# Performance work log

Hardware: AMD Instinct MI355X
Metric: run time of the kernel (lower is better)

Reference implementation:

```python
import jax, jax.numpy as jnp
import numpy as np

N = 10000       # nodes
E = 640000      # edges (before self-loops)
D_IN = 128
H1 = 128
H2 = 64
EMB = 64
NEG_SLOPE = 0.2  # PyG GATConv default


def setup_inputs() -> dict:
    key = jax.random.key(0)
    ks = jax.random.split(key, 12)
    s = 0.05
    return {
        "x": jax.random.normal(ks[0], (N, D_IN), dtype=jnp.float32),
        "edge_index": jax.random.randint(ks[1], (2, E), 0, N, dtype=jnp.int64),
        "W1": jax.random.normal(ks[2], (D_IN, H1), dtype=jnp.float32) * s,
        "a_src1": jax.random.normal(ks[3], (H1,), dtype=jnp.float32) * s,
        "a_dst1": jax.random.normal(ks[4], (H1,), dtype=jnp.float32) * s,
        "b1": jnp.zeros((H1,), dtype=jnp.float32),
        "W2": jax.random.normal(ks[5], (H1, H2), dtype=jnp.float32) * s,
        "a_src2": jax.random.normal(ks[6], (H2,), dtype=jnp.float32) * s,
        "a_dst2": jax.random.normal(ks[7], (H2,), dtype=jnp.float32) * s,
        "b2": jnp.zeros((H2,), dtype=jnp.float32),
        "Wp": jax.random.normal(ks[8], (H2, EMB), dtype=jnp.float32) * s,
        "bp": jnp.zeros((EMB,), dtype=jnp.float32),
    }


def _gat_conv(x, src, dst, W, a_src, a_dst, b):
    # x: [N, Din] -> h: [N, Dout]
    h = x @ W
    # edge-wise attention logits (PyG: alpha_src from source j, alpha_dst from target i)
    logits = jax.nn.leaky_relu((h @ a_src)[src] + (h @ a_dst)[dst], NEG_SLOPE)  # [E+N]
    # softmax over incoming edges of each destination node (numerically stable)
    m = jax.ops.segment_max(logits, dst, num_segments=N)
    e = jnp.exp(logits - m[dst])
    z = jax.ops.segment_sum(e, dst, num_segments=N)
    w = e / z[dst]                                                              # [E+N]
    # weighted scatter-add of source features into destinations
    out = jax.ops.segment_sum(w[:, None] * h[src], dst, num_segments=N)         # [N, Dout]
    return out + b


def reference(x, edge_index, W1, a_src1, a_dst1, b1, W2, a_src2, a_dst2, b2, Wp, bp):
    # add self-loops (PyG GATConv default add_self_loops=True)
    loop = jnp.arange(N, dtype=edge_index.dtype)
    ei = jnp.concatenate([edge_index, jnp.stack([loop, loop])], axis=1)
    src, dst = ei[0], ei[1]
    x1 = jax.nn.relu(_gat_conv(x, src, dst, W1, a_src1, a_dst1, b1))
    x2 = jax.nn.relu(_gat_conv(x1, src, dst, W2, a_src2, a_dst2, b2))
    return x2 @ Wp + bp  # [N, EMB]
```

## Files before the change

kernel.cpp:

```cpp
#include <hip/hip_runtime.h>
#include <hip/hip_bf16.h>

#define NNODES 10000
#define NEDGES 640000
#define NTOT   (NNODES + NEDGES)
#define D_IN 128
#define H1 128
#define H2 64
#define EMB 64

#define NBUCKET 160
#define BCAP    8192
#define CHUNK   4096


__global__ __launch_bounds__(256) void bucket_kernel(const int* __restrict__ ei,
                                                     int* __restrict__ bucket_cursor,
                                                     int* __restrict__ bucket_arr) {
    __shared__ int ordered[CHUNK];
    __shared__ int hist[NBUCKET];
    __shared__ int binStart[NBUCKET];
    __shared__ int bincur[NBUCKET];
    __shared__ int gcur[NBUCKET];
    __shared__ int wtmp[4];

    int tid = threadIdx.x;
    int base = blockIdx.x * CHUNK;
    int n = NTOT - base; if (n > CHUNK) n = CHUNK;

    int rec[CHUNK / 256];
#pragma unroll
    for (int k = 0; k < CHUNK / 256; ++k) {
        int i = base + k * 256 + tid;
        int r = 0;
        if (i < NTOT) {
            int s, d;
            if (i < NEDGES) { s = ei[i]; d = ei[NEDGES + i]; }
            else            { s = d = i - NEDGES; }
            r = (d << 16) | s;
        }
        rec[k] = r;
    }

    for (int b = tid; b < NBUCKET; b += 256) hist[b] = 0;
    __syncthreads();
#pragma unroll
    for (int k = 0; k < CHUNK / 256; ++k) {
        int i = base + k * 256 + tid;
        if (i < NTOT) atomicAdd(&hist[rec[k] >> 22], 1);
    }
    __syncthreads();

    {
        int v = (tid < NBUCKET) ? hist[tid] : 0;
        int lane = tid & 63, w = tid >> 6;
        int inc = v;
        for (int o = 1; o < 64; o <<= 1) {
            int t = __shfl_up(inc, o, 64);
            if (lane >= o) inc += t;
        }
        if (lane == 63) wtmp[w] = inc;
        __syncthreads();
        int pre = 0;
        for (int i = 0; i < w; ++i) pre += wtmp[i];
        if (tid < NBUCKET) {
            binStart[tid] = pre + inc - v;
            bincur[tid]   = pre + inc - v;
        }
    }
    __syncthreads();

#pragma unroll
    for (int k = 0; k < CHUNK / 256; ++k) {
        int i = base + k * 256 + tid;
        if (i < NTOT) {
            int pos = atomicAdd(&bincur[rec[k] >> 22], 1);
            ordered[pos] = rec[k];
        }
    }
    __syncthreads();

    for (int b = tid; b < NBUCKET; b += 256) {
        int c = hist[b];
        gcur[b] = c ? atomicAdd(&bucket_cursor[b], c) : 0;
    }
    __syncthreads();

#pragma unroll
    for (int k = 0; k < CHUNK / 256; ++k) {
        int i = k * 256 + tid;
        if (i < n) {
            int r = ordered[i];
            int b = r >> 22;
            bucket_arr[b * BCAP + gcur[b] + (i - binStart[b])] = r;
        }
    }
}

__global__ __launch_bounds__(256) void bucket_scan_kernel(const int* __restrict__ bucket_cursor,
                                                          int* __restrict__ bucket_base) {
    __shared__ int wtmp[4];
    int tid = threadIdx.x;
    int v = (tid < NBUCKET) ? bucket_cursor[tid] : 0;
    int lane = tid & 63, w = tid >> 6;
    int inc = v;
    for (int o = 1; o < 64; o <<= 1) {
        int t = __shfl_up(inc, o, 64);
        if (lane >= o) inc += t;
    }
    if (lane == 63) wtmp[w] = inc;
    __syncthreads();
    int pre = 0;
    for (int i = 0; i < w; ++i) pre += wtmp[i];
    if (tid < NBUCKET) bucket_base[tid] = pre + inc - v;
}


__global__ __launch_bounds__(256) void build_kernel(const int* __restrict__ bucket_cursor,
                                                    const int* __restrict__ bucket_base,
                                                    const int* __restrict__ bucket_arr,
                                                    int* __restrict__ rowptr,
                                                    int* __restrict__ csr_src) {
    __shared__ int hist[64];
    __shared__ int bincur[64];
    int tid = threadIdx.x;
    int b = blockIdx.x;
    int cnt = bucket_cursor[b];
    int base = bucket_base[b];
    const int* arr = bucket_arr + b * BCAP;

    if (tid < 64) hist[tid] = 0;
    __syncthreads();
    for (int i = tid; i < cnt; i += 256) atomicAdd(&hist[(arr[i] >> 16) & 63], 1);
    __syncthreads();

    if (tid < 64) {
        int v = hist[tid];
        int inc = v;
        for (int o = 1; o < 64; o <<= 1) {
            int t = __shfl_up(inc, o, 64);
            if (tid >= o) inc += t;
        }
        bincur[tid] = inc - v;
        int node = b * 64 + tid;
        if (node < NNODES) rowptr[node] = base + inc - v;
    }
    if (b == 0 && tid == 0) rowptr[NNODES] = NTOT;
    __syncthreads();

    for (int i = tid; i < cnt; i += 256) {
        int r = arr[i];
        int pos = base + atomicAdd(&bincur[(r >> 16) & 63], 1);
        csr_src[pos] = r & 0xFFFF;
    }
}


template <int K, int NC, bool BIAS, bool DOTS>
__global__ __launch_bounds__(256) void gemm_kernel(const float* __restrict__ A,
                                                   const float* __restrict__ B,
                                                   const float* __restrict__ bias,
                                                   float* __restrict__ C, int M,
                                                   const float* __restrict__ a_src,
                                                   const float* __restrict__ a_dst,
                                                   float* __restrict__ as,
                                                   float* __restrict__ ad) {
    __shared__ float Alds[32 * K];
    __shared__ float Blds[K * NC];
    int tid = threadIdx.x;
    int row0 = blockIdx.x * 32;

    const float4* A4 = (const float4*)(A + (size_t)row0 * K);
    float4* Al4 = (float4*)Alds;
    constexpr int A4N = 32 * K / 4;
    for (int idx = tid; idx < A4N; idx += 256) {
        int r = idx / (K / 4);
        float4 z4 = {0.f, 0.f, 0.f, 0.f};
        Al4[idx] = (row0 + r < M) ? A4[idx] : z4;
    }
    const float4* B4 = (const float4*)B;
    float4* Bl4 = (float4*)Blds;
    constexpr int B4N = K * NC / 4;
    for (int idx = tid; idx < B4N; idx += 256) Bl4[idx] = B4[idx];
    __syncthreads();

    int tx = tid & 31;
    int ty = tid >> 5;
    constexpr int CPT = NC / 32;
    float acc[4][CPT];
#pragma unroll
    for (int rr = 0; rr < 4; ++rr)
#pragma unroll
        for (int cc = 0; cc < CPT; ++cc) acc[rr][cc] = 0.f;

    for (int k = 0; k < K; ++k) {
        float bv[CPT];
        const float* Bk = &Blds[k * NC + tx * CPT];
#pragma unroll
        for (int cc = 0; cc < CPT; ++cc) bv[cc] = Bk[cc];
#pragma unroll
        for (int rr = 0; rr < 4; ++rr) {
            float a = Alds[(ty + 8 * rr) * K + k];
#pragma unroll
            for (int cc = 0; cc < CPT; ++cc) acc[rr][cc] = fmaf(a, bv[cc], acc[rr][cc]);
        }
    }

#pragma unroll
    for (int rr = 0; rr < 4; ++rr) {
        int gr = row0 + ty + 8 * rr;
        if (gr < M) {
#pragma unroll
            for (int cc = 0; cc < CPT; ++cc) {
                int c = tx * CPT + cc;
                float v = acc[rr][cc];
                if (BIAS) v += bias[c];
                C[(size_t)gr * NC + c] = v;
            }
        }
    }

    if (DOTS) {
        float asv[CPT], adv[CPT];
#pragma unroll
        for (int cc = 0; cc < CPT; ++cc) {
            asv[cc] = a_src[tx * CPT + cc];
            adv[cc] = a_dst[tx * CPT + cc];
        }
#pragma unroll
        for (int rr = 0; rr < 4; ++rr) {
            float s1 = 0.f, s2 = 0.f;
#pragma unroll
            for (int cc = 0; cc < CPT; ++cc) {
                s1 = fmaf(acc[rr][cc], asv[cc], s1);
                s2 = fmaf(acc[rr][cc], adv[cc], s2);
            }
#pragma unroll
            for (int o = 1; o < 32; o <<= 1) {
                s1 += __shfl_xor(s1, o, 64);
                s2 += __shfl_xor(s2, o, 64);
            }
            int gr = row0 + ty + 8 * rr;
            if (tx == 0 && gr < M) { as[gr] = s1; ad[gr] = s2; }
        }
    }
}


template <int H>
__global__ __launch_bounds__(256) void agg_kernel(const int* __restrict__ rowptr,
                                                  const int* __restrict__ csr_src,
                                                  const float* __restrict__ h,
                                                  const float* __restrict__ as,
                                                  const float* __restrict__ ad,
                                                  const float* __restrict__ bias,
                                                  float* __restrict__ out) {
    int wid = (blockIdx.x * blockDim.x + threadIdx.x) >> 6;
    int lane = threadIdx.x & 63;
    if (wid >= NNODES) return;
    int beg = rowptr[wid];
    int end = rowptr[wid + 1];
    float ad_d = ad[wid];

    const float2* h2 = (const float2*)h;
    float z = 0.f, acc0 = 0.f, acc1 = 0.f;

    for (int chunk = beg; chunk < end; chunk += 64) {
        int myj = chunk + lane;
        int cnt = end - chunk; if (cnt > 64) cnt = 64;
        int s_l = 0;
        float e_l = 0.f;
        if (myj < end) {
            s_l = csr_src[myj];
            float l = as[s_l] + ad_d;
            l = (l > 0.f) ? l : 0.2f * l;
            e_l = __expf(l);
        }
        z += e_l;
        int cnt4 = (cnt + 3) & ~3;
        for (int t = 0; t < cnt4; t += 4) {
#pragma unroll
            for (int u = 0; u < 4; ++u) {
                int tt = __builtin_amdgcn_readfirstlane(t + u);
                int s = __builtin_amdgcn_readlane(s_l, tt);
                float e = __int_as_float(
                    __builtin_amdgcn_readlane(__float_as_int(e_l), tt));
                if (H == 128) {
                    float2 v = h2[(size_t)s * 64 + lane];
                    acc0 = fmaf(e, v.x, acc0);
                    acc1 = fmaf(e, v.y, acc1);
                } else {
                    float v = h[(size_t)s * H + lane];
                    acc0 = fmaf(e, v, acc0);
                }
            }
        }
    }
    for (int o = 32; o; o >>= 1) z += __shfl_xor(z, o, 64);
    float rz = 1.f / z;
    if (H == 128) {
        float2 bb = ((const float2*)bias)[lane];
        float2 o2;
        o2.x = fmaxf(acc0 * rz + bb.x, 0.f);
        o2.y = fmaxf(acc1 * rz + bb.y, 0.f);
        ((float2*)out)[(size_t)wid * 64 + lane] = o2;
    } else {
        float o0 = fmaxf(acc0 * rz + bias[lane], 0.f);
        out[(size_t)wid * H + lane] = o0;
    }
}


extern "C" void kernel_launch(void* const* d_in, const int* in_sizes, int n_in,
                              void* d_out, int out_size, void* d_ws, size_t ws_size,
                              hipStream_t stream) {
    const float* x      = (const float*)d_in[0];
    const int*   ei     = (const int*)d_in[1];
    const float* W1     = (const float*)d_in[2];
    const float* a_src1 = (const float*)d_in[3];
    const float* a_dst1 = (const float*)d_in[4];
    const float* b1     = (const float*)d_in[5];
    const float* W2     = (const float*)d_in[6];
    const float* a_src2 = (const float*)d_in[7];
    const float* a_dst2 = (const float*)d_in[8];
    const float* b2     = (const float*)d_in[9];
    const float* Wp     = (const float*)d_in[10];
    const float* bp     = (const float*)d_in[11];
    float* out = (float*)d_out;

    char* ws = (char*)d_ws;
    size_t off = 0;
    auto alloc = [&](size_t bytes) {
        void* p = ws + off;
        off = (off + bytes + 255) & ~(size_t)255;
        return p;
    };
    int*   bucket_cursor = (int*)alloc(NBUCKET * 4);
    int*   bucket_base   = (int*)alloc(NBUCKET * 4);
    int*   bucket_arr    = (int*)alloc((size_t)NBUCKET * BCAP * 4);
    int*   rowptr  = (int*)alloc((NNODES + 1) * 4);
    int*   csr_src = (int*)alloc((size_t)NTOT * 4);
    float* h1      = (float*)alloc((size_t)NNODES * H1 * 4);
    float* as1     = (float*)alloc(NNODES * 4);
    float* ad1     = (float*)alloc(NNODES * 4);
    float* x1      = (float*)alloc((size_t)NNODES * H1 * 4);
    float* h2      = (float*)alloc((size_t)NNODES * H2 * 4);
    float* as2     = (float*)alloc(NNODES * 4);
    float* ad2     = (float*)alloc(NNODES * 4);
    float* x2      = (float*)alloc((size_t)NNODES * H2 * 4);
    (void)ws_size;

    const int TB = 256;
    int gemm_b = (NNODES + 31) / 32;
    int wave_b = (NNODES * 64 + TB - 1) / TB;
    int p1_b = (NTOT + CHUNK - 1) / CHUNK;

    hipMemsetAsync(bucket_cursor, 0, NBUCKET * 4, stream);
    bucket_kernel<<<p1_b, TB, 0, stream>>>(ei, bucket_cursor, bucket_arr);
    bucket_scan_kernel<<<1, TB, 0, stream>>>(bucket_cursor, bucket_base);
    build_kernel<<<NBUCKET - 3, TB, 0, stream>>>(bucket_cursor, bucket_base,
                                                 bucket_arr, rowptr, csr_src);

    gemm_kernel<D_IN, H1, false, true><<<gemm_b, TB, 0, stream>>>(
        x, W1, nullptr, h1, NNODES, a_src1, a_dst1, as1, ad1);
    agg_kernel<H1><<<wave_b, TB, 0, stream>>>(rowptr, csr_src, h1, as1, ad1, b1, x1);

    gemm_kernel<H1, H2, false, true><<<gemm_b, TB, 0, stream>>>(
        x1, W2, nullptr, h2, NNODES, a_src2, a_dst2, as2, ad2);
    agg_kernel<H2><<<wave_b, TB, 0, stream>>>(rowptr, csr_src, h2, as2, ad2, b2, x2);

    gemm_kernel<H2, EMB, true, false><<<gemm_b, TB, 0, stream>>>(
        x2, Wp, bp, out, NNODES, nullptr, nullptr, nullptr, nullptr);
}
```

Before: 184.3 us.

## Fuse all stages into one persistent kernel with grid-wide barriers

Replaces the chain of separate launches (bucket, scan, build, three GEMMs, two aggregations) with one persistent 256-block kernel that uses atomic grid barriers between phases. The first layer's GEMM runs on spare blocks at the same time as edge bucketing, and the bucket scan is folded into the build phase. GEMM tiles now stream K in 64-wide slices so all phases can share one shared-memory union. This removes launch gaps and tail effects, but limits parallelism to 256 blocks, relies on all blocks being co-resident for the spin barriers, and shared-memory use may lower occupancy.

```diff
diff --git a/kernel.cpp b/kernel.cpp
--- a/kernel.cpp
+++ b/kernel.cpp
@@ -12,20 +12,45 @@
 #define NBUCKET 160
 #define BCAP    8192
 #define CHUNK   4096
-
-
-__global__ __launch_bounds__(256) void bucket_kernel(const int* __restrict__ ei,
-                                                     int* __restrict__ bucket_cursor,
-                                                     int* __restrict__ bucket_arr) {
-    __shared__ int ordered[CHUNK];
-    __shared__ int hist[NBUCKET];
-    __shared__ int binStart[NBUCKET];
-    __shared__ int bincur[NBUCKET];
-    __shared__ int gcur[NBUCKET];
-    __shared__ int wtmp[4];
-
+#define NCHUNK  ((NTOT + CHUNK - 1) / CHUNK)
+#define NTILE   ((NNODES + 31) / 32)
+#define NBBLK   ((NNODES + 63) / 64)
+#define GRID    256
+#define TB      256
+
+struct Params {
+    const float* x; const int* ei;
+    const float* W1; const float* a_src1; const float* a_dst1; const float* b1;
+    const float* W2; const float* a_src2; const float* a_dst2; const float* b2;
+    const float* Wp; const float* bp;
+    float* out;
+    int* bar; int* bucket_cursor; int* bucket_arr; int* rowptr; int* csr_src;
+    float* h1; float* as1; float* ad1; float* x1;
+    float* h2; float* as2; float* ad2; float* x2;
+};
+
+union SMem {
+    struct { int ordered[CHUNK]; int hist[NBUCKET]; int binStart[NBUCKET];
+             int bincur[NBUCKET]; int gcur[NBUCKET]; int wtmp[4]; } p1;
+    struct { int base[NBUCKET]; int wtmp[4]; int hist[64]; int bincur[64]; } p2;
+    struct { float A[32 * 64]; float B[64 * 128]; } g;
+};
+
+__device__ __forceinline__ void gridbar(int* __restrict__ bar, int k) {
+    __syncthreads();
+    if (threadIdx.x == 0) {
+        __hip_atomic_fetch_add(&bar[k], 1, __ATOMIC_RELEASE, __HIP_MEMORY_SCOPE_AGENT);
+        while (__hip_atomic_load(&bar[k], __ATOMIC_ACQUIRE, __HIP_MEMORY_SCOPE_AGENT) < GRID)
+            __builtin_amdgcn_s_sleep(2);
+    }
+    __syncthreads();
+}
+
+__device__ __forceinline__ void bucket_chunk(SMem& sm, int c, const int* __restrict__ ei,
+                                             int* __restrict__ bucket_cursor,
+                                             int* __restrict__ bucket_arr) {
     int tid = threadIdx.x;
-    int base = blockIdx.x * CHUNK;
+    int base = c * CHUNK;
     int n = NTOT - base; if (n > CHUNK) n = CHUNK;
 
     int rec[CHUNK / 256];
@@ -42,30 +67,30 @@
         rec[k] = r;
     }
 
-    for (int b = tid; b < NBUCKET; b += 256) hist[b] = 0;
+    for (int b = tid; b < NBUCKET; b += 256) sm.p1.hist[b] = 0;
     __syncthreads();
 #pragma unroll
     for (int k = 0; k < CHUNK / 256; ++k) {
         int i = base + k * 256 + tid;
-        if (i < NTOT) atomicAdd(&hist[rec[k] >> 22], 1);
+        if (i < NTOT) atomicAdd(&sm.p1.hist[rec[k] >> 22], 1);
     }
     __syncthreads();
 
     {
-        int v = (tid < NBUCKET) ? hist[tid] : 0;
+        int v = (tid < NBUCKET) ? sm.p1.hist[tid] : 0;
         int lane = tid & 63, w = tid >> 6;
         int inc = v;
         for (int o = 1; o < 64; o <<= 1) {
             int t = __shfl_up(inc, o, 64);
             if (lane >= o) inc += t;
         }
-        if (lane == 63) wtmp[w] = inc;
+        if (lane == 63) sm.p1.wtmp[w] = inc;
         __syncthreads();
         int pre = 0;
-        for (int i = 0; i < w; ++i) pre += wtmp[i];
+        for (int i = 0; i < w; ++i) pre += sm.p1.wtmp[i];
         if (tid < NBUCKET) {
-            binStart[tid] = pre + inc - v;
-            bincur[tid]   = pre + inc - v;
+            sm.p1.binStart[tid] = pre + inc - v;
+            sm.p1.bincur[tid]   = pre + inc - v;
         }
     }
     __syncthreads();
@@ -74,15 +99,15 @@
     for (int k = 0; k < CHUNK / 256; ++k) {
         int i = base + k * 256 + tid;
         if (i < NTOT) {
-            int pos = atomicAdd(&bincur[rec[k] >> 22], 1);
-            ordered[pos] = rec[k];
+            int pos = atomicAdd(&sm.p1.bincur[rec[k] >> 22], 1);
+            sm.p1.ordered[pos] = rec[k];
         }
     }
     __syncthreads();
 
     for (int b = tid; b < NBUCKET; b += 256) {
-        int c = hist[b];
-        gcur[b] = c ? atomicAdd(&bucket_cursor[b], c) : 0;
+        int cc = sm.p1.hist[b];
+        sm.p1.gcur[b] = cc ? atomicAdd(&bucket_cursor[b], cc) : 0;
     }
     __syncthreads();
 
@@ -90,58 +115,51 @@
     for (int k = 0; k < CHUNK / 256; ++k) {
         int i = k * 256 + tid;
         if (i < n) {
-            int r = ordered[i];
+            int r = sm.p1.ordered[i];
             int b = r >> 22;
-            bucket_arr[b * BCAP + gcur[b] + (i - binStart[b])] = r;
-        }
-    }
-}
-
-__global__ __launch_bounds__(256) void bucket_scan_kernel(const int* __restrict__ bucket_cursor,
-                                                          int* __restrict__ bucket_base) {
-    __shared__ int wtmp[4];
+            bucket_arr[b * BCAP + sm.p1.gcur[b] + (i - sm.p1.binStart[b])] = r;
+        }
+    }
+}
+
+__device__ __forceinline__ void build_bucket(SMem& sm, int b,
+                                             const int* __restrict__ bucket_cursor,
+                                             const int* __restrict__ bucket_arr,
+                                             int* __restrict__ rowptr,
+                                             int* __restrict__ csr_src) {
     int tid = threadIdx.x;
-    int v = (tid < NBUCKET) ? bucket_cursor[tid] : 0;
-    int lane = tid & 63, w = tid >> 6;
-    int inc = v;
-    for (int o = 1; o < 64; o <<= 1) {
-        int t = __shfl_up(inc, o, 64);
-        if (lane >= o) inc += t;
-    }
-    if (lane == 63) wtmp[w] = inc;
-    __syncthreads();
-    int pre = 0;
-    for (int i = 0; i < w; ++i) pre += wtmp[i];
-    if (tid < NBUCKET) bucket_base[tid] = pre + inc - v;
-}
-
-
-__global__ __launch_bounds__(256) void build_kernel(const int* __restrict__ bucket_cursor,
-                                                    const int* __restrict__ bucket_base,
-                                                    const int* __restrict__ bucket_arr,
-                                                    int* __restrict__ rowptr,
-                                                    int* __restrict__ csr_src) {
-    __shared__ int hist[64];
-    __shared__ int bincur[64];
-    int tid = threadIdx.x;
-    int b = blockIdx.x;
+    {
+        int v = (tid < NBUCKET) ? bucket_cursor[tid] : 0;
+        int lane = tid & 63, w = tid >> 6;
+        int inc = v;
+        for (int o = 1; o < 64; o <<= 1) {
+            int t = __shfl_up(inc, o, 64);
+            if (lane >= o) inc += t;
+        }
+        if (lane == 63) sm.p2.wtmp[w] = inc;
+        __syncthreads();
+        int pre = 0;
+        for (int i = 0; i < w; ++i) pre += sm.p2.wtmp[i];
+        if (tid < NBUCKET) sm.p2.base[tid] = pre + inc - v;
+    }
+    __syncthreads();
     int cnt = bucket_cursor[b];
-    int base = bucket_base[b];
+    int base = sm.p2.base[b];
     const int* arr = bucket_arr + b * BCAP;
 
-    if (tid < 64) hist[tid] = 0;
-    __syncthreads();
-    for (int i = tid; i < cnt; i += 256) atomicAdd(&hist[(arr[i] >> 16) & 63], 1);
+    if (tid < 64) sm.p2.hist[tid] = 0;
+    __syncthreads();
+    for (int i = tid; i < cnt; i += 256) atomicAdd(&sm.p2.hist[(arr[i] >> 16) & 63], 1);
     __syncthreads();
 
     if (tid < 64) {
-        int v = hist[tid];
+        int v = sm.p2.hist[tid];
         int inc = v;
         for (int o = 1; o < 64; o <<= 1) {
             int t = __shfl_up(inc, o, 64);
             if (tid >= o) inc += t;
         }
-        bincur[tid] = inc - v;
+        sm.p2.bincur[tid] = inc - v;
         int node = b * 64 + tid;
         if (node < NNODES) rowptr[node] = base + inc - v;
     }
@@ -150,40 +168,23 @@
 
     for (int i = tid; i < cnt; i += 256) {
         int r = arr[i];
-        int pos = base + atomicAdd(&bincur[(r >> 16) & 63], 1);
+        int pos = base + atomicAdd(&sm.p2.bincur[(r >> 16) & 63], 1);
         csr_src[pos] = r & 0xFFFF;
     }
 }
 
-
 template <int K, int NC, bool BIAS, bool DOTS>
-__global__ __launch_bounds__(256) void gemm_kernel(const float* __restrict__ A,
-                                                   const float* __restrict__ B,
-                                                   const float* __restrict__ bias,
-                                                   float* __restrict__ C, int M,
-                                                   const float* __restrict__ a_src,
-                                                   const float* __restrict__ a_dst,
-                                                   float* __restrict__ as,
-                                                   float* __restrict__ ad) {
-    __shared__ float Alds[32 * K];
-    __shared__ float Blds[K * NC];
+__device__ __forceinline__ void gemm_tile(SMem& sm, int t,
+                                          const float* __restrict__ A,
+                                          const float* __restrict__ B,
+                                          const float* __restrict__ bias,
+                                          float* __restrict__ C,
+                                          const float* __restrict__ a_src,
+                                          const float* __restrict__ a_dst,
+                                          float* __restrict__ as,
+                                          float* __restrict__ ad) {
     int tid = threadIdx.x;
-    int row0 = blockIdx.x * 32;
-
-    const float4* A4 = (const float4*)(A + (size_t)row0 * K);
-    float4* Al4 = (float4*)Alds;
-    constexpr int A4N = 32 * K / 4;
-    for (int idx = tid; idx < A4N; idx += 256) {
-        int r = idx / (K / 4);
-        float4 z4 = {0.f, 0.f, 0.f, 0.f};
-        Al4[idx] = (row0 + r < M) ? A4[idx] : z4;
-    }
-    const float4* B4 = (const float4*)B;
-    float4* Bl4 = (float4*)Blds;
-    constexpr int B4N = K * NC / 4;
-    for (int idx = tid; idx < B4N; idx += 256) Bl4[idx] = B4[idx];
-    __syncthreads();
-
+    int row0 = t * 32;
     int tx = tid & 31;
     int ty = tid >> 5;
     constexpr int CPT = NC / 32;
@@ -193,23 +194,38 @@
 #pragma unroll
         for (int cc = 0; cc < CPT; ++cc) acc[rr][cc] = 0.f;
 
-    for (int k = 0; k < K; ++k) {
-        float bv[CPT];
-        const float* Bk = &Blds[k * NC + tx * CPT];
-#pragma unroll
-        for (int cc = 0; cc < CPT; ++cc) bv[cc] = Bk[cc];
-#pragma unroll
-        for (int rr = 0; rr < 4; ++rr) {
-            float a = Alds[(ty + 8 * rr) * K + k];
-#pragma unroll
-            for (int cc = 0; cc < CPT; ++cc) acc[rr][cc] = fmaf(a, bv[cc], acc[rr][cc]);
-        }
+    for (int kk = 0; kk < K; kk += 64) {
+        float4* Al4 = (float4*)sm.g.A;
+        const float4* A4 = (const float4*)(A + (size_t)row0 * K + kk);
+        for (int idx = tid; idx < 32 * 16; idx += 256) {
+            int r = idx >> 4, c = idx & 15;
+            float4 z4 = {0.f, 0.f, 0.f, 0.f};
+            Al4[idx] = (row0 + r < NNODES) ? A4[r * (K / 4) + c] : z4;
+        }
+        float4* Bl4 = (float4*)sm.g.B;
+        const float4* B4 = (const float4*)(B + (size_t)kk * NC);
+        for (int idx = tid; idx < 64 * NC / 4; idx += 256) Bl4[idx] = B4[idx];
+        __syncthreads();
+
+        for (int k = 0; k < 64; ++k) {
+            float bv[CPT];
+            const float* Bk = &sm.g.B[k * NC + tx * CPT];
+#pragma unroll
+            for (int cc = 0; cc < CPT; ++cc) bv[cc] = Bk[cc];
+#pragma unroll
+            for (int rr = 0; rr < 4; ++rr) {
+                float a = sm.g.A[(ty + 8 * rr) * 64 + k];
+#pragma unroll
+                for (int cc = 0; cc < CPT; ++cc) acc[rr][cc] = fmaf(a, bv[cc], acc[rr][cc]);
+            }
+        }
+        __syncthreads();
     }
 
 #pragma unroll
     for (int rr = 0; rr < 4; ++rr) {
         int gr = row0 + ty + 8 * rr;
-        if (gr < M) {
+        if (gr < NNODES) {
 #pragma unroll
             for (int cc = 0; cc < CPT; ++cc) {
                 int c = tx * CPT + cc;
@@ -241,93 +257,113 @@
                 s2 += __shfl_xor(s2, o, 64);
             }
             int gr = row0 + ty + 8 * rr;
-            if (tx == 0 && gr < M) { as[gr] = s1; ad[gr] = s2; }
-        }
-    }
-}
-
+            if (tx == 0 && gr < NNODES) { as[gr] = s1; ad[gr] = s2; }
+        }
+    }
+}
 
 template <int H>
-__global__ __launch_bounds__(256) void agg_kernel(const int* __restrict__ rowptr,
-                                                  const int* __restrict__ csr_src,
-                                                  const float* __restrict__ h,
-                                                  const float* __restrict__ as,
-                                                  const float* __restrict__ ad,
-                                                  const float* __restrict__ bias,
-                                                  float* __restrict__ out) {
-    int wid = (blockIdx.x * blockDim.x + threadIdx.x) >> 6;
+__device__ __forceinline__ void agg_nodes(const int* __restrict__ rowptr,
+                                          const int* __restrict__ csr_src,
+                                          const float* __restrict__ h,
+                                          const float* __restrict__ as,
+                                          const float* __restrict__ ad,
+                                          const float* __restrict__ bias,
+                                          float* __restrict__ out) {
+    int gw = (blockIdx.x * blockDim.x + threadIdx.x) >> 6;
+    int nw = (GRID * TB) >> 6;
     int lane = threadIdx.x & 63;
-    if (wid >= NNODES) return;
-    int beg = rowptr[wid];
-    int end = rowptr[wid + 1];
-    float ad_d = ad[wid];
-
     const float2* h2 = (const float2*)h;
-    float z = 0.f, acc0 = 0.f, acc1 = 0.f;
-
-    for (int chunk = beg; chunk < end; chunk += 64) {
-        int myj = chunk + lane;
-        int cnt = end - chunk; if (cnt > 64) cnt = 64;
-        int s_l = 0;
-        float e_l = 0.f;
-        if (myj < end) {
-            s_l = csr_src[myj];
-            float l = as[s_l] + ad_d;
-            l = (l > 0.f) ? l : 0.2f * l;
-            e_l = __expf(l);
-        }
-        z += e_l;
-        int cnt4 = (cnt + 3) & ~3;
-        for (int t = 0; t < cnt4; t += 4) {
-#pragma unroll
-            for (int u = 0; u < 4; ++u) {
-                int tt = __builtin_amdgcn_readfirstlane(t + u);
-                int s = __builtin_amdgcn_readlane(s_l, tt);
-                float e = __int_as_float(
-                    __builtin_amdgcn_readlane(__float_as_int(e_l), tt));
-                if (H == 128) {
-                    float2 v = h2[(size_t)s * 64 + lane];
-                    acc0 = fmaf(e, v.x, acc0);
-                    acc1 = fmaf(e, v.y, acc1);
-                } else {
-                    float v = h[(size_t)s * H + lane];
-                    acc0 = fmaf(e, v, acc0);
+
+    for (int wid = gw; wid < NNODES; wid += nw) {
+        int beg = rowptr[wid];
+        int end = rowptr[wid + 1];
+        float ad_d = ad[wid];
+        float z = 0.f, acc0 = 0.f, acc1 = 0.f;
+
+        for (int chunk = beg; chunk < end; chunk += 64) {
+            int myj = chunk + lane;
+            int cnt = end - chunk; if (cnt > 64) cnt = 64;
+            int s_l = 0;
+            float e_l = 0.f;
+            if (myj < end) {
+                s_l = csr_src[myj];
+                float l = as[s_l] + ad_d;
+                l = (l > 0.f) ? l : 0.2f * l;
+                e_l = __expf(l);
+            }
+            z += e_l;
+            int cnt4 = (cnt + 3) & ~3;
+            for (int t = 0; t < cnt4; t += 4) {
+#pragma unroll
+                for (int u = 0; u < 4; ++u) {
+                    int tt = __builtin_amdgcn_readfirstlane(t + u);
+                    int s = __builtin_amdgcn_readlane(s_l, tt);
+                    float e = __int_as_float(
+                        __builtin_amdgcn_readlane(__float_as_int(e_l), tt));
+                    if (H == 128) {
+                        float2 v = h2[(size_t)s * 64 + lane];
+                        acc0 = fmaf(e, v.x, acc0);
+                        acc1 = fmaf(e, v.y, acc1);
+                    } else {
+                        float v = h[(size_t)s * H + lane];
+                        acc0 = fmaf(e, v, acc0);
+                    }
                 }
             }
         }
-    }
-    for (int o = 32; o; o >>= 1) z += __shfl_xor(z, o, 64);
-    float rz = 1.f / z;
-    if (H == 128) {
-        float2 bb = ((const float2*)bias)[lane];
-        float2 o2;
-        o2.x = fmaxf(acc0 * rz + bb.x, 0.f);
-        o2.y = fmaxf(acc1 * rz + bb.y, 0.f);
-        ((float2*)out)[(size_t)wid * 64 + lane] = o2;
+        for (int o = 32; o; o >>= 1) z += __shfl_xor(z, o, 64);
+        float rz = 1.f / z;
+        if (H == 128) {
+            float2 bb = ((const float2*)bias)[lane];
+            float2 o2;
+            o2.x = fmaxf(acc0 * rz + bb.x, 0.f);
+            o2.y = fmaxf(acc1 * rz + bb.y, 0.f);
+            ((float2*)out)[(size_t)wid * 64 + lane] = o2;
+        } else {
+            float o0 = fmaxf(acc0 * rz + bias[lane], 0.f);
+            out[(size_t)wid * H + lane] = o0;
+        }
+    }
+}
+
+__global__ __launch_bounds__(TB) void mega(Params p) {
+    __shared__ SMem sm;
+    int bid = blockIdx.x;
+
+    if (bid < NCHUNK) {
+        bucket_chunk(sm, bid, p.ei, p.bucket_cursor, p.bucket_arr);
     } else {
-        float o0 = fmaxf(acc0 * rz + bias[lane], 0.f);
-        out[(size_t)wid * H + lane] = o0;
-    }
+        for (int t = bid - NCHUNK; t < NTILE; t += GRID - NCHUNK)
+            gemm_tile<D_IN, H1, false, true>(sm, t, p.x, p.W1, nullptr, p.h1,
+                                             p.a_src1, p.a_dst1, p.as1, p.ad1);
+    }
+    gridbar(p.bar, 0);
+
+    if (bid < NBBLK)
+        build_bucket(sm, bid, p.bucket_cursor, p.bucket_arr, p.rowptr, p.csr_src);
+    gridbar(p.bar, 1);
+
+    agg_nodes<H1>(p.rowptr, p.csr_src, p.h1, p.as1, p.ad1, p.b1, p.x1);
+    gridbar(p.bar, 2);
+
+    for (int t = bid; t < NTILE; t += GRID)
+        gemm_tile<H1, H2, false, true>(sm, t, p.x1, p.W2, nullptr, p.h2,
+                                       p.a_src2, p.a_dst2, p.as2, p.ad2);
+    gridbar(p.bar, 3);
+
+    agg_nodes<H2>(p.rowptr, p.csr_src, p.h2, p.as2, p.ad2, p.b2, p.x2);
+    gridbar(p.bar, 4);
+
+    for (int t = bid; t < NTILE; t += GRID)
+        gemm_tile<H2, EMB, true, false>(sm, t, p.x2, p.Wp, p.bp, p.out,
+                                        nullptr, nullptr, nullptr, nullptr);
 }
 
 
 extern "C" void kernel_launch(void* const* d_in, const int* in_sizes, int n_in,
                               void* d_out, int out_size, void* d_ws, size_t ws_size,
                               hipStream_t stream) {
-    const float* x      = (const float*)d_in[0];
-    const int*   ei     = (const int*)d_in[1];
-    const float* W1     = (const float*)d_in[2];
-    const float* a_src1 = (const float*)d_in[3];
-    const float* a_dst1 = (const float*)d_in[4];
-    const float* b1     = (const float*)d_in[5];
-    const float* W2     = (const float*)d_in[6];
-    const float* a_src2 = (const float*)d_in[7];
-    const float* a_dst2 = (const float*)d_in[8];
-    const float* b2     = (const float*)d_in[9];
-    const float* Wp     = (const float*)d_in[10];
-    const float* bp     = (const float*)d_in[11];
-    float* out = (float*)d_out;
-
     char* ws = (char*)d_ws;
     size_t off = 0;
     auto alloc = [&](size_t bytes) {
@@ -335,40 +371,38 @@
         off = (off + bytes + 255) & ~(size_t)255;
         return p;
     };
-    int*   bucket_cursor = (int*)alloc(NBUCKET * 4);
-    int*   bucket_base   = (int*)alloc(NBUCKET * 4);
-    int*   bucket_arr    = (int*)alloc((size_t)NBUCKET * BCAP * 4);
-    int*   rowptr  = (int*)alloc((NNODES + 1) * 4);
-    int*   csr_src = (int*)alloc((size_t)NTOT * 4);
-    float* h1      = (float*)alloc((size_t)NNODES * H1 * 4);
-    float* as1     = (float*)alloc(NNODES * 4);
-    float* ad1     = (float*)alloc(NNODES * 4);
-    float* x1      = (float*)alloc((size_t)NNODES * H1 * 4);
-    float* h2      = (float*)alloc((size_t)NNODES * H2 * 4);
-    float* as2     = (float*)alloc(NNODES * 4);
-    float* ad2     = (float*)alloc(NNODES * 4);
-    float* x2      = (float*)alloc((size_t)NNODES * H2 * 4);
-    (void)ws_size;
-
-    const int TB = 256;
-    int gemm_b = (NNODES + 31) / 32;
-    int wave_b = (NNODES * 64 + TB - 1) / TB;
-    int p1_b = (NTOT + CHUNK - 1) / CHUNK;
-
-    hipMemsetAsync(bucket_cursor, 0, NBUCKET * 4, stream);
-    bucket_kernel<<<p1_b, TB, 0, stream>>>(ei, bucket_cursor, bucket_arr);
-    bucket_scan_kernel<<<1, TB, 0, stream>>>(bucket_cursor, bucket_base);
-    build_kernel<<<NBUCKET - 3, TB, 0, stream>>>(bucket_cursor, bucket_base,
-                                                 bucket_arr, rowptr, csr_src);
-
-    gemm_kernel<D_IN, H1, false, true><<<gemm_b, TB, 0, stream>>>(
-        x, W1, nullptr, h1, NNODES, a_src1, a_dst1, as1, ad1);
-    agg_kernel<H1><<<wave_b, TB, 0, stream>>>(rowptr, csr_src, h1, as1, ad1, b1, x1);
-
-    gemm_kernel<H1, H2, false, true><<<gemm_b, TB, 0, stream>>>(
-        x1, W2, nullptr, h2, NNODES, a_src2, a_dst2, as2, ad2);
-    agg_kernel<H2><<<wave_b, TB, 0, stream>>>(rowptr, csr_src, h2, as2, ad2, b2, x2);
-
-    gemm_kernel<H2, EMB, true, false><<<gemm_b, TB, 0, stream>>>(
-        x2, Wp, bp, out, NNODES, nullptr, nullptr, nullptr, nullptr);
-}
+
+    Params p;
+    p.x      = (const float*)d_in[0];
+    p.ei     = (const int*)d_in[1];
+    p.W1     = (const float*)d_in[2];
+    p.a_src1 = (const float*)d_in[3];
+    p.a_dst1 = (const float*)d_in[4];
+    p.b1     = (const float*)d_in[5];
+    p.W2     = (const float*)d_in[6];
+    p.a_src2 = (const float*)d_in[7];
+    p.a_dst2 = (const float*)d_in[8];
+    p.b2     = (const float*)d_in[9];
+    p.Wp     = (const float*)d_in[10];
+    p.bp     = (const float*)d_in[11];
+    p.out    = (float*)d_out;
+
+    p.bar           = (int*)alloc(16 * 4);
+    p.bucket_cursor = (int*)alloc(NBUCKET * 4);
+    size_t zero_bytes = off;
+    p.bucket_arr    = (int*)alloc((size_t)NBUCKET * BCAP * 4);
+    p.rowptr        = (int*)alloc((NNODES + 1) * 4);
+    p.csr_src       = (int*)alloc((size_t)NTOT * 4);
+    p.h1            = (float*)alloc((size_t)NNODES * H1 * 4);
+    p.as1           = (float*)alloc(NNODES * 4);
+    p.ad1           = (float*)alloc(NNODES * 4);
+    p.x1            = (float*)alloc((size_t)NNODES * H1 * 4);
+    p.h2            = (float*)alloc((size_t)NNODES * H2 * 4);
+    p.as2           = (float*)alloc(NNODES * 4);
+    p.ad2           = (float*)alloc(NNODES * 4);
+    p.x2            = (float*)alloc((size_t)NNODES * H2 * 4);
+    (void)ws_size; (void)in_sizes; (void)n_in; (void)out_size;
+
+    hipMemsetAsync(d_ws, 0, zero_bytes, stream);
+    mega<<<GRID, TB, 0, stream>>>(p);
+}
```

Measured after the change: 502.2 us. 172% more time.
